# Kernel optimization log

Measured on AMD Instinct MI355X. Metric: run time of the kernel, lower is better.

Reference implementation:

```python
import jax, jax.numpy as jnp
import numpy as np

N = 100000   # nodes
E = 1000000  # edges (before self-loops)
G = 64       # graphs in batch
IN, HID, OUT = 128, 64, 1


def setup_inputs() -> dict:
    key = jax.random.key(0)
    ks = jax.random.split(key, 24)
    inp = {
        "x": jax.random.normal(ks[0], (N, IN), jnp.float32),
        "adj": jax.random.randint(ks[1], (2, E), 0, N, jnp.int32),
        "batch": jnp.sort(jax.random.randint(ks[2], (N,), 0, G, jnp.int32)),
    }
    i = 3
    dims = [(IN, HID), (HID, HID), (HID, HID)]
    for l, (di, do) in enumerate(dims, start=1):
        inp[f"W{l}"] = jax.random.normal(ks[i], (di, do), jnp.float32) * (1.0 / np.sqrt(di)); i += 1
        inp[f"a_src{l}"] = jax.random.normal(ks[i], (do,), jnp.float32) * 0.1; i += 1
        inp[f"a_dst{l}"] = jax.random.normal(ks[i], (do,), jnp.float32) * 0.1; i += 1
        inp[f"b{l}"] = jnp.zeros((do,), jnp.float32); i += 1
    inp["linnews_W"] = jax.random.normal(ks[i], (IN, HID), jnp.float32) * (1.0 / np.sqrt(IN)); i += 1
    inp["linnews_b"] = jnp.zeros((HID,), jnp.float32)
    inp["lin0_W"] = jax.random.normal(ks[i], (HID, HID), jnp.float32) * (1.0 / np.sqrt(HID)); i += 1
    inp["lin0_b"] = jnp.zeros((HID,), jnp.float32)
    inp["lin1_W"] = jax.random.normal(ks[i], (2 * HID, OUT), jnp.float32) * (1.0 / np.sqrt(2 * HID)); i += 1
    inp["lin1_b"] = jnp.zeros((OUT,), jnp.float32)
    return inp


def _gat_layer(x, src, dst, W, a_src, a_dst, b):
    # PyG GATConv, heads=1, self-loops already appended to (src, dst).
    h = x @ W                                        # [N, HID]
    e = (h @ a_src)[src] + (h @ a_dst)[dst]          # [E'] edge scores
    e = jax.nn.leaky_relu(e, 0.2)
    # segment softmax over incoming edges of each dst node
    m = jax.ops.segment_max(e, dst, num_segments=N)
    num = jnp.exp(e - m[dst])
    den = jax.ops.segment_sum(num, dst, num_segments=N)
    coef = num / (den[dst] + 1e-16)                  # [E']
    out = jax.ops.segment_sum(coef[:, None] * h[src], dst, num_segments=N)
    return out + b


def reference(x, adj, batch, W1, a_src1, a_dst1, b1, W2, a_src2, a_dst2, b2,
              W3, a_src3, a_dst3, b3, linnews_W, linnews_b, lin0_W, lin0_b,
              lin1_W, lin1_b):
    loop = jnp.arange(N, dtype=adj.dtype)
    src = jnp.concatenate([adj[0], loop])
    dst = jnp.concatenate([adj[1], loop])

    h = jax.nn.relu(_gat_layer(x, src, dst, W1, a_src1, a_dst1, b1))
    h = jax.nn.relu(_gat_layer(h, src, dst, W2, a_src2, a_dst2, b2))
    h = jax.nn.relu(_gat_layer(h, src, dst, W3, a_src3, a_dst3, b3))

    # global max pool per graph
    h = jax.ops.segment_max(h, batch, num_segments=G)        # [G, HID]
    h = jax.nn.relu(h @ lin0_W + lin0_b)

    # root node of each graph = first index with that batch id
    root = jax.ops.segment_min(jnp.arange(N), batch, num_segments=G)  # [G]
    news = jax.nn.relu(x[root] @ linnews_W + linnews_b)      # [G, HID]

    out = jnp.concatenate([h, news], axis=-1) @ lin1_W + lin1_b
    return jax.nn.sigmoid(out)                               # [G, 1]
```

## Files before the change

### kernel.cpp

```cpp
#include <hip/hip_runtime.h>
#include <hip/hip_fp16.h>
#include <cstdint>
#include <type_traits>

#define THREADS 256
#define NBLK 64
#define BPAD 512
#define LINBLK 640

typedef _Float16 half8 __attribute__((ext_vector_type(8)));
typedef float v4f __attribute__((ext_vector_type(4)));

__global__ __launch_bounds__(256) void hist_kernel(const int* __restrict__ dst_e,
                                                   int* __restrict__ hist, int E, int chunk,
                                                   float* __restrict__ pool, int* __restrict__ root,
                                                   int G) {
  __shared__ int hcnt[BPAD];
  int t = threadIdx.x, blk = blockIdx.x;
  if (blk == 0) {
    for (int i = t; i < G * 64; i += 256) pool[i] = 0.0f;
    for (int i = t; i < G; i += 256) root[i] = 0x7fffffff;
  }
  for (int i = t; i < BPAD; i += 256) hcnt[i] = 0;
  __syncthreads();
  int s = blk * chunk, e = s + chunk;
  if (e > E) e = E;
  for (int i = s + t; i < e; i += 256) atomicAdd(&hcnt[dst_e[i] >> 8], 1);
  __syncthreads();
  for (int b = t; b < BPAD; b += 256) hist[b * NBLK + blk] = hcnt[b];
}

__global__ __launch_bounds__(256) void hscan_kernel(int* __restrict__ hist) {
  __shared__ int part[256];
  const int PER = (BPAD * NBLK) / 256;
  int t = threadIdx.x;
  int base = t * PER;
  int sum = 0;
  for (int k = 0; k < PER; k++) sum += hist[base + k];
  part[t] = sum;
  __syncthreads();
  int own = sum;
  for (int off = 1; off < 256; off <<= 1) {
    int v = (t >= off) ? part[t - off] : 0;
    __syncthreads();
    part[t] += v;
    __syncthreads();
  }
  int run = part[t] - own;
  for (int k = 0; k < PER; k++) {
    int h = hist[base + k];
    hist[base + k] = run;
    run += h;
  }
}

__global__ __launch_bounds__(256) void scatter_kernel(const int* __restrict__ src_e,
                                                      const int* __restrict__ dst_e,
                                                      const int* __restrict__ hist,
                                                      unsigned int* __restrict__ ebuf,
                                                      int E, int chunk) {
  __shared__ int cur[BPAD];
  int t = threadIdx.x, blk = blockIdx.x;
  for (int b = t; b < BPAD; b += 256) cur[b] = hist[b * NBLK + blk];
  __syncthreads();
  int s = blk * chunk, e = s + chunk;
  if (e > E) e = E;
  for (int i = s + t; i < e; i += 256) {
    int d = dst_e[i];
    unsigned int sv = (unsigned int)src_e[i];
    int slot = atomicAdd(&cur[d >> 8], 1);
    ebuf[slot] = (sv << 8) | (unsigned int)(d & 255);
  }
}

__global__ __launch_bounds__(256) void build_kernel(const unsigned int* __restrict__ ebuf,
                                                    const int* __restrict__ hist,
                                                    int* __restrict__ row_start,
                                                    int* __restrict__ csr_src,
                                                    int N, int E) {
  __shared__ int counts[256];
  __shared__ int sc[256];
  __shared__ int curw[256];
  int t = threadIdx.x, b = blockIdx.x;
  int nbase = b * 256;
  int ebase = hist[b * NBLK];
  int eend = hist[(b + 1) * NBLK];
  counts[t] = 0;
  __syncthreads();
  int ecount = eend - ebase;
  for (int i = t; i < ecount; i += 256)
    atomicAdd(&counts[ebuf[ebase + i] & 255u], 1);
  __syncthreads();
  int n = nbase + t;
  int val = (n < N) ? counts[t] + 1 : 0;
  sc[t] = val;
  __syncthreads();
  int own = val;
  for (int off = 1; off < 256; off <<= 1) {
    int v = (t >= off) ? sc[t - off] : 0;
    __syncthreads();
    sc[t] += v;
    __syncthreads();
  }
  int myloc = sc[t] - own;
  int rowb = ebase + nbase;
  if (n < N) {
    row_start[n] = rowb + myloc;
    csr_src[rowb + myloc + counts[t]] = n;
    if (n == N - 1) row_start[N] = rowb + myloc + counts[t] + 1;
  }
  curw[t] = rowb + myloc;
  __syncthreads();
  for (int i = t; i < ecount; i += 256) {
    unsigned int ev = ebuf[ebase + i];
    int pos = atomicAdd(&curw[ev & 255u], 1);
    csr_src[pos] = (int)(ev >> 8);
  }
}

template <int K, typename TIN>
__global__ __launch_bounds__(256) void lin_attn_kernel(
    const TIN* __restrict__ in, const float* __restrict__ W,
    const float* __restrict__ a_src, const float* __restrict__ a_dst,
    __half2* __restrict__ h2, float* __restrict__ as_, float* __restrict__ ad_,
    int N, int nwaves) {
  constexpr int NKC = K / 32;
  __shared__ _Float16 sh[4][16 * 64];
  const int t = threadIdx.x;
  const int lane = t & 63, w = t >> 6;
  const int col = lane & 15, quad = lane >> 4;
  const int wid = blockIdx.x * 4 + w;

  half8 bf[4][NKC];
#pragma unroll
  for (int nt = 0; nt < 4; nt++)
#pragma unroll
    for (int kc = 0; kc < NKC; kc++) {
      half8 v;
#pragma unroll
      for (int j = 0; j < 8; j++)
        v[j] = (_Float16)W[(kc * 32 + quad * 8 + j) * 64 + nt * 16 + col];
      bf[nt][kc] = v;
    }
  float sa[4], sd[4];
#pragma unroll
  for (int nt = 0; nt < 4; nt++) {
    sa[nt] = a_src[nt * 16 + col];
    sd[nt] = a_dst[nt * 16 + col];
  }

  const int ntiles = (N + 15) >> 4;
  for (int tile = wid; tile < ntiles; tile += nwaves) {
    const int nb = tile << 4;
    int nodeA = nb + col;
    if (nodeA >= N) nodeA = N - 1;
    const TIN* arow = in + (size_t)nodeA * K + quad * 8;

    v4f acc[4];
#pragma unroll
    for (int nt = 0; nt < 4; nt++) acc[nt] = (v4f){0.f, 0.f, 0.f, 0.f};

#pragma unroll
    for (int kc = 0; kc < NKC; kc++) {
      half8 a;
      if constexpr (std::is_same<TIN, float>::value) {
        float4 f0 = *(const float4*)(arow + kc * 32);
        float4 f1 = *(const float4*)(arow + kc * 32 + 4);
        a[0] = (_Float16)f0.x; a[1] = (_Float16)f0.y;
        a[2] = (_Float16)f0.z; a[3] = (_Float16)f0.w;
        a[4] = (_Float16)f1.x; a[5] = (_Float16)f1.y;
        a[6] = (_Float16)f1.z; a[7] = (_Float16)f1.w;
      } else {
        a = *(const half8*)(arow + kc * 32);
      }
#pragma unroll
      for (int nt = 0; nt < 4; nt++)
        acc[nt] = __builtin_amdgcn_mfma_f32_16x16x32_f16(a, bf[nt][kc], acc[nt], 0, 0, 0);
    }

    float ps[4], pd[4];
#pragma unroll
    for (int r = 0; r < 4; r++) { ps[r] = 0.f; pd[r] = 0.f; }
#pragma unroll
    for (int nt = 0; nt < 4; nt++)
#pragma unroll
      for (int r = 0; r < 4; r++) {
        ps[r] += acc[nt][r] * sa[nt];
        pd[r] += acc[nt][r] * sd[nt];
      }
#pragma unroll
    for (int r = 0; r < 4; r++)
#pragma unroll
      for (int m = 1; m < 16; m <<= 1) {
        ps[r] += __shfl_xor(ps[r], m);
        pd[r] += __shfl_xor(pd[r], m);
      }
    if (col == 0) {
#pragma unroll
      for (int r = 0; r < 4; r++) {
        int node = nb + quad * 4 + r;
        if (node < N) { as_[node] = ps[r]; ad_[node] = pd[r]; }
      }
    }

#pragma unroll
    for (int nt = 0; nt < 4; nt++)
#pragma unroll
      for (int r = 0; r < 4; r++)
        sh[w][(quad * 4 + r) * 64 + nt * 16 + col] = (_Float16)acc[nt][r];
    int nr = lane >> 2, c4 = lane & 3;
    float4 v0 = *(float4*)&sh[w][nr * 64 + c4 * 16];
    float4 v1 = *(float4*)&sh[w][nr * 64 + c4 * 16 + 8];
    int node = nb + nr;
    if (node < N) {
      *(float4*)&h2[(size_t)node * 32 + c4 * 8] = v0;
      *(float4*)&h2[(size_t)node * 32 + c4 * 8 + 4] = v1;
    }
  }
}

__global__ __launch_bounds__(256) void agg_kernel(
    const __half2* __restrict__ h2, const float* __restrict__ as_, const float* __restrict__ ad_,
    const int* __restrict__ csr_src, const int* __restrict__ row_start,
    const float* __restrict__ b, _Float16* __restrict__ out16, int N) {
  int t = threadIdx.x;
  int lane = t & 63, w = t >> 6;
  int ng = lane >> 3, co = lane & 7;
  int n = blockIdx.x * 32 + w * 8 + ng;
  if (n >= N) return;
  int rs = row_start[n], re = row_start[n + 1];
  float adn = ad_[n];
  const float4* h4 = (const float4*)h2;

  float4 A0 = make_float4(0.f, 0.f, 0.f, 0.f);
  float4 A1 = make_float4(0.f, 0.f, 0.f, 0.f);
  float den = 0.f;
  for (int s = rs; s < re; s += 4) {
    int src[4];
#pragma unroll
    for (int j = 0; j < 4; j++) {
      int sj = s + j;
      src[j] = csr_src[(sj < re) ? sj : (re - 1)];
    }
    float cf[4];
#pragma unroll
    for (int j = 0; j < 4; j++) {
      float e = as_[src[j]] + adn;
      e = fmaxf(e, 0.2f * e);
      cf[j] = (s + j < re) ? __expf(e) : 0.f;
    }
#pragma unroll
    for (int j = 0; j < 4; j++) {
      float4 hv = h4[(size_t)src[j] * 8 + co];
      const __half2* hp = (const __half2*)&hv;
      float2 f0 = __half22float2(hp[0]);
      float2 f1 = __half22float2(hp[1]);
      float2 f2 = __half22float2(hp[2]);
      float2 f3 = __half22float2(hp[3]);
      float c = cf[j];
      den += c;
      A0.x += c * f0.x; A0.y += c * f0.y; A0.z += c * f1.x; A0.w += c * f1.y;
      A1.x += c * f2.x; A1.y += c * f2.y; A1.z += c * f3.x; A1.w += c * f3.y;
    }
  }
  float inv = 1.0f / (den + 1e-16f);
  float4 b0 = *(const float4*)&b[co * 8];
  float4 b1 = *(const float4*)&b[co * 8 + 4];
  _Float16 o[8];
  o[0] = (_Float16)fmaxf(A0.x * inv + b0.x, 0.f);
  o[1] = (_Float16)fmaxf(A0.y * inv + b0.y, 0.f);
  o[2] = (_Float16)fmaxf(A0.z * inv + b0.z, 0.f);
  o[3] = (_Float16)fmaxf(A0.w * inv + b0.w, 0.f);
  o[4] = (_Float16)fmaxf(A1.x * inv + b1.x, 0.f);
  o[5] = (_Float16)fmaxf(A1.y * inv + b1.y, 0.f);
  o[6] = (_Float16)fmaxf(A1.z * inv + b1.z, 0.f);
  o[7] = (_Float16)fmaxf(A1.w * inv + b1.w, 0.f);
  *(float4*)&out16[(size_t)n * 64 + co * 8] = *(float4*)o;
}

__global__ void pool_kernel(const _Float16* __restrict__ h, const int* __restrict__ batch,
                            float* __restrict__ pool, int* __restrict__ root,
                            int N, int chunk) {
  int t = threadIdx.x;
  int lane = t & 63, w = t >> 6;
  int row = blockIdx.x * 4 + w;
  int start = row * chunk;
  if (start >= N) return;
  int end = start + chunk; if (end > N) end = N;
  int cur_g = batch[start];
  if (lane == 0 && (start == 0 || batch[start - 1] != cur_g)) atomicMin(&root[cur_g], start);
  float rm = 0.0f;
  for (int n = start; n < end; n++) {
    int g = batch[n];
    if (g != cur_g) {
      atomicMax((int*)&pool[(size_t)cur_g * 64 + lane], __float_as_int(rm));
      if (lane == 0) atomicMin(&root[g], n);
      cur_g = g;
      rm = 0.0f;
    }
    rm = fmaxf(rm, (float)h[(size_t)n * 64 + lane]);
  }
  atomicMax((int*)&pool[(size_t)cur_g * 64 + lane], __float_as_int(rm));
}

__global__ void final_kernel(const float* __restrict__ pool, const int* __restrict__ root,
                             const float* __restrict__ x,
                             const float* __restrict__ lin0_W, const float* __restrict__ lin0_b,
                             const float* __restrict__ linnews_W, const float* __restrict__ linnews_b,
                             const float* __restrict__ lin1_W, const float* __restrict__ lin1_b,
                             float* __restrict__ out, int G, int N) {
  int t = threadIdx.x;
  int lane = t & 63, w = t >> 6;
  int g = blockIdx.x * 4 + w;
  if (g >= G) return;
  float hp = 0.f;
  for (int k = 0; k < 64; k++) hp += pool[(size_t)g * 64 + k] * lin0_W[k * 64 + lane];
  hp = fmaxf(hp + lin0_b[lane], 0.f);
  int r = root[g]; if (r > N - 1) r = N - 1; if (r < 0) r = 0;
  float nw = 0.f;
  for (int k = 0; k < 128; k++) nw += x[(size_t)r * 128 + k] * linnews_W[k * 64 + lane];
  nw = fmaxf(nw + linnews_b[lane], 0.f);
  float p = hp * lin1_W[lane] + nw * lin1_W[64 + lane];
  for (int k = 1; k < 64; k <<= 1) p += __shfl_xor(p, k);
  if (lane == 0) out[g] = 1.0f / (1.0f + __expf(-(p + lin1_b[0])));
}

extern "C" void kernel_launch(void* const* d_in, const int* in_sizes, int n_in,
                              void* d_out, int out_size, void* d_ws, size_t ws_size,
                              hipStream_t stream) {
  (void)n_in; (void)ws_size;
  const float* x      = (const float*)d_in[0];
  const int*   adj    = (const int*)d_in[1];
  const int*   batch  = (const int*)d_in[2];
  const float* W1     = (const float*)d_in[3];
  const float* asrc1  = (const float*)d_in[4];
  const float* adst1  = (const float*)d_in[5];
  const float* b1     = (const float*)d_in[6];
  const float* W2     = (const float*)d_in[7];
  const float* asrc2  = (const float*)d_in[8];
  const float* adst2  = (const float*)d_in[9];
  const float* b2     = (const float*)d_in[10];
  const float* W3     = (const float*)d_in[11];
  const float* asrc3  = (const float*)d_in[12];
  const float* adst3  = (const float*)d_in[13];
  const float* b3     = (const float*)d_in[14];
  const float* lnW    = (const float*)d_in[15];
  const float* lnb    = (const float*)d_in[16];
  const float* l0W    = (const float*)d_in[17];
  const float* l0b    = (const float*)d_in[18];
  const float* l1W    = (const float*)d_in[19];
  const float* l1b    = (const float*)d_in[20];
  float* outp = (float*)d_out;

  const int N = in_sizes[2];
  const int E = in_sizes[1] / 2;
  const int Etot = E + N;
  const int G = out_size;
  const int B = (N + 255) / 256;

  const int* src_e = adj;
  const int* dst_e = adj + E;

  uintptr_t p = (uintptr_t)d_ws;
  auto alloc = [&](size_t bytes) -> void* {
    void* r = (void*)p;
    p += (bytes + 255) & ~(size_t)255;
    return r;
  };
  int*      hist      = (int*)alloc((size_t)BPAD * NBLK * 4);
  int*      row_start = (int*)alloc((size_t)(N + 1) * 4);
  int*      csr_src   = (int*)alloc((size_t)Etot * 4);
  unsigned int* ebuf  = (unsigned int*)alloc((size_t)E * 4);
  __half2*  hbufL     = (__half2*)alloc((size_t)N * 32 * 4);
  _Float16* hbufA     = (_Float16*)alloc((size_t)N * 64 * 2);
  float*    as_       = (float*)alloc((size_t)N * 4);
  float*    ad_       = (float*)alloc((size_t)N * 4);
  float*    pool      = (float*)alloc((size_t)G * 64 * 4);
  int*      root      = (int*)alloc((size_t)G * 4);

  int chunk = (E + NBLK - 1) / NBLK;
  hist_kernel<<<dim3(NBLK), dim3(256), 0, stream>>>(dst_e, hist, E, chunk, pool, root, G);
  hscan_kernel<<<dim3(1), dim3(256), 0, stream>>>(hist);
  scatter_kernel<<<dim3(NBLK), dim3(256), 0, stream>>>(src_e, dst_e, hist, ebuf, E, chunk);
  build_kernel<<<dim3(B), dim3(256), 0, stream>>>(ebuf, hist, row_start, csr_src, N, E);

  const int aggGrid = (N + 31) / 32;
  const int nwaves = LINBLK * 4;

  lin_attn_kernel<128, float><<<dim3(LINBLK), dim3(256), 0, stream>>>(
      x, W1, asrc1, adst1, hbufL, as_, ad_, N, nwaves);
  agg_kernel<<<dim3(aggGrid), dim3(256), 0, stream>>>(hbufL, as_, ad_, csr_src, row_start, b1, hbufA, N);
  lin_attn_kernel<64, _Float16><<<dim3(LINBLK), dim3(256), 0, stream>>>(
      hbufA, W2, asrc2, adst2, hbufL, as_, ad_, N, nwaves);
  agg_kernel<<<dim3(aggGrid), dim3(256), 0, stream>>>(hbufL, as_, ad_, csr_src, row_start, b2, hbufA, N);
  lin_attn_kernel<64, _Float16><<<dim3(LINBLK), dim3(256), 0, stream>>>(
      hbufA, W3, asrc3, adst3, hbufL, as_, ad_, N, nwaves);
  agg_kernel<<<dim3(aggGrid), dim3(256), 0, stream>>>(hbufL, as_, ad_, csr_src, row_start, b3, hbufA, N);

  const int ROWS = 2048;
  int pchunk = (N + ROWS - 1) / ROWS;
  pool_kernel<<<dim3(ROWS / 4), dim3(256), 0, stream>>>(hbufA, batch, pool, root, N, pchunk);

  final_kernel<<<dim3((G + 3) / 4), dim3(256), 0, stream>>>(
      pool, root, x, l0W, l0b, lnW, lnb, l1W, l1b, outp, G, N);
}
```

Before: 325.2 us.

## Fuse GAT aggregation with next layer's linear+attention and final pooling

After: 309.4 us. 4.9% less time.

```diff
diff --git a/kernel.cpp b/kernel.cpp
--- a/kernel.cpp
+++ b/kernel.cpp
@@ -125,7 +125,7 @@
     __half2* __restrict__ h2, float* __restrict__ as_, float* __restrict__ ad_,
     int N, int nwaves) {
   constexpr int NKC = K / 32;
-  __shared__ _Float16 sh[4][16 * 64];
+  __shared__ _Float16 sh[4][16 * 72];
   const int t = threadIdx.x;
   const int lane = t & 63, w = t >> 6;
   const int col = lane & 15, quad = lane >> 4;
@@ -207,10 +207,10 @@
     for (int nt = 0; nt < 4; nt++)
 #pragma unroll
       for (int r = 0; r < 4; r++)
-        sh[w][(quad * 4 + r) * 64 + nt * 16 + col] = (_Float16)acc[nt][r];
+        sh[w][(quad * 4 + r) * 72 + nt * 16 + col] = (_Float16)acc[nt][r];
     int nr = lane >> 2, c4 = lane & 3;
-    float4 v0 = *(float4*)&sh[w][nr * 64 + c4 * 16];
-    float4 v1 = *(float4*)&sh[w][nr * 64 + c4 * 16 + 8];
+    float4 v0 = *(float4*)&sh[w][nr * 72 + c4 * 16];
+    float4 v1 = *(float4*)&sh[w][nr * 72 + c4 * 16 + 8];
     int node = nb + nr;
     if (node < N) {
       *(float4*)&h2[(size_t)node * 32 + c4 * 8] = v0;
@@ -219,22 +219,11 @@
   }
 }
 
-__global__ __launch_bounds__(256) void agg_kernel(
-    const __half2* __restrict__ h2, const float* __restrict__ as_, const float* __restrict__ ad_,
-    const int* __restrict__ csr_src, const int* __restrict__ row_start,
-    const float* __restrict__ b, _Float16* __restrict__ out16, int N) {
-  int t = threadIdx.x;
-  int lane = t & 63, w = t >> 6;
-  int ng = lane >> 3, co = lane & 7;
-  int n = blockIdx.x * 32 + w * 8 + ng;
-  if (n >= N) return;
-  int rs = row_start[n], re = row_start[n + 1];
-  float adn = ad_[n];
-  const float4* h4 = (const float4*)h2;
-
-  float4 A0 = make_float4(0.f, 0.f, 0.f, 0.f);
-  float4 A1 = make_float4(0.f, 0.f, 0.f, 0.f);
-  float den = 0.f;
+__device__ __forceinline__ void agg_node(const float4* __restrict__ h4,
+                                         const float* __restrict__ as_in, float adn,
+                                         const int* __restrict__ csr_src,
+                                         int rs, int re, int co,
+                                         float4& A0, float4& A1, float& den) {
   for (int s = rs; s < re; s += 4) {
     int src[4];
 #pragma unroll
@@ -245,7 +234,7 @@
     float cf[4];
 #pragma unroll
     for (int j = 0; j < 4; j++) {
-      float e = as_[src[j]] + adn;
+      float e = as_in[src[j]] + adn;
       e = fmaxf(e, 0.2f * e);
       cf[j] = (s + j < re) ? __expf(e) : 0.f;
     }
@@ -263,44 +252,179 @@
       A1.x += c * f2.x; A1.y += c * f2.y; A1.z += c * f3.x; A1.w += c * f3.y;
     }
   }
+}
+
+__global__ __launch_bounds__(256) void agg_lin_kernel(
+    const __half2* __restrict__ h2in, const float* __restrict__ as_in,
+    const float* __restrict__ ad_in, const int* __restrict__ csr_src,
+    const int* __restrict__ row_start, const float* __restrict__ bprev,
+    const float* __restrict__ W, const float* __restrict__ a_src,
+    const float* __restrict__ a_dst, __half2* __restrict__ h2out,
+    float* __restrict__ as_out, float* __restrict__ ad_out, int N) {
+  __shared__ _Float16 shh[32][72];
+  __shared__ _Float16 sht[2][16 * 72];
+  const int t = threadIdx.x;
+  const int lane = t & 63, w = t >> 6;
+
+  {
+    const int ng = lane >> 3, co = lane & 7;
+    const int ln = w * 8 + ng;
+    int n = blockIdx.x * 32 + ln;
+    int nc = (n < N) ? n : (N - 1);
+    int rs = row_start[nc], re = row_start[nc + 1];
+    float adn = ad_in[nc];
+    const float4* h4 = (const float4*)h2in;
+    float4 A0 = make_float4(0.f, 0.f, 0.f, 0.f);
+    float4 A1 = make_float4(0.f, 0.f, 0.f, 0.f);
+    float den = 0.f;
+    agg_node(h4, as_in, adn, csr_src, rs, re, co, A0, A1, den);
+    float inv = 1.0f / (den + 1e-16f);
+    float4 b0 = *(const float4*)&bprev[co * 8];
+    float4 b1 = *(const float4*)&bprev[co * 8 + 4];
+    _Float16 o[8];
+    o[0] = (_Float16)fmaxf(A0.x * inv + b0.x, 0.f);
+    o[1] = (_Float16)fmaxf(A0.y * inv + b0.y, 0.f);
+    o[2] = (_Float16)fmaxf(A0.z * inv + b0.z, 0.f);
+    o[3] = (_Float16)fmaxf(A0.w * inv + b0.w, 0.f);
+    o[4] = (_Float16)fmaxf(A1.x * inv + b1.x, 0.f);
+    o[5] = (_Float16)fmaxf(A1.y * inv + b1.y, 0.f);
+    o[6] = (_Float16)fmaxf(A1.z * inv + b1.z, 0.f);
+    o[7] = (_Float16)fmaxf(A1.w * inv + b1.w, 0.f);
+    *(float4*)&shh[ln][co * 8] = *(float4*)o;
+  }
+  __syncthreads();
+  if (w >= 2) return;
+
+  const int col = lane & 15, quad = lane >> 4;
+  half8 bf[4][2];
+  float sa[4], sd[4];
+#pragma unroll
+  for (int nt = 0; nt < 4; nt++) {
+#pragma unroll
+    for (int kc = 0; kc < 2; kc++) {
+      half8 v;
+#pragma unroll
+      for (int j = 0; j < 8; j++)
+        v[j] = (_Float16)W[(kc * 32 + quad * 8 + j) * 64 + nt * 16 + col];
+      bf[nt][kc] = v;
+    }
+    sa[nt] = a_src[nt * 16 + col];
+    sd[nt] = a_dst[nt * 16 + col];
+  }
+
+  const int nb = blockIdx.x * 32 + w * 16;
+  v4f acc[4];
+#pragma unroll
+  for (int nt = 0; nt < 4; nt++) acc[nt] = (v4f){0.f, 0.f, 0.f, 0.f};
+#pragma unroll
+  for (int kc = 0; kc < 2; kc++) {
+    half8 a = *(const half8*)&shh[w * 16 + col][kc * 32 + quad * 8];
+#pragma unroll
+    for (int nt = 0; nt < 4; nt++)
+      acc[nt] = __builtin_amdgcn_mfma_f32_16x16x32_f16(a, bf[nt][kc], acc[nt], 0, 0, 0);
+  }
+
+  float ps[4], pd[4];
+#pragma unroll
+  for (int r = 0; r < 4; r++) { ps[r] = 0.f; pd[r] = 0.f; }
+#pragma unroll
+  for (int nt = 0; nt < 4; nt++)
+#pragma unroll
+    for (int r = 0; r < 4; r++) {
+      ps[r] += acc[nt][r] * sa[nt];
+      pd[r] += acc[nt][r] * sd[nt];
+    }
+#pragma unroll
+  for (int r = 0; r < 4; r++)
+#pragma unroll
+    for (int m = 1; m < 16; m <<= 1) {
+      ps[r] += __shfl_xor(ps[r], m);
+      pd[r] += __shfl_xor(pd[r], m);
+    }
+  if (col == 0) {
+#pragma unroll
+    for (int r = 0; r < 4; r++) {
+      int node = nb + quad * 4 + r;
+      if (node < N) { as_out[node] = ps[r]; ad_out[node] = pd[r]; }
+    }
+  }
+
+#pragma unroll
+  for (int nt = 0; nt < 4; nt++)
+#pragma unroll
+    for (int r = 0; r < 4; r++)
+      sht[w][(quad * 4 + r) * 72 + nt * 16 + col] = (_Float16)acc[nt][r];
+  int nr = lane >> 2, c4 = lane & 3;
+  float4 v0 = *(float4*)&sht[w][nr * 72 + c4 * 16];
+  float4 v1 = *(float4*)&sht[w][nr * 72 + c4 * 16 + 8];
+  int node = nb + nr;
+  if (node < N) {
+    *(float4*)&h2out[(size_t)node * 32 + c4 * 8] = v0;
+    *(float4*)&h2out[(size_t)node * 32 + c4 * 8 + 4] = v1;
+  }
+}
+
+__global__ __launch_bounds__(256) void agg_pool_kernel(
+    const __half2* __restrict__ h2in, const float* __restrict__ as_in,
+    const float* __restrict__ ad_in, const int* __restrict__ csr_src,
+    const int* __restrict__ row_start, const float* __restrict__ bprev,
+    const int* __restrict__ batch, float* __restrict__ pool,
+    int* __restrict__ root, int N) {
+  __shared__ float red[4][64];
+  const int t = threadIdx.x;
+  const int lane = t & 63, w = t >> 6;
+  const int ng = lane >> 3, co = lane & 7;
+  const int ln = w * 8 + ng;
+  int n = blockIdx.x * 32 + ln;
+  int nc = (n < N) ? n : (N - 1);
+  int rs = row_start[nc], re = row_start[nc + 1];
+  float adn = ad_in[nc];
+  const float4* h4 = (const float4*)h2in;
+  float4 A0 = make_float4(0.f, 0.f, 0.f, 0.f);
+  float4 A1 = make_float4(0.f, 0.f, 0.f, 0.f);
+  float den = 0.f;
+  agg_node(h4, as_in, adn, csr_src, rs, re, co, A0, A1, den);
   float inv = 1.0f / (den + 1e-16f);
-  float4 b0 = *(const float4*)&b[co * 8];
-  float4 b1 = *(const float4*)&b[co * 8 + 4];
-  _Float16 o[8];
-  o[0] = (_Float16)fmaxf(A0.x * inv + b0.x, 0.f);
-  o[1] = (_Float16)fmaxf(A0.y * inv + b0.y, 0.f);
-  o[2] = (_Float16)fmaxf(A0.z * inv + b0.z, 0.f);
-  o[3] = (_Float16)fmaxf(A0.w * inv + b0.w, 0.f);
-  o[4] = (_Float16)fmaxf(A1.x * inv + b1.x, 0.f);
-  o[5] = (_Float16)fmaxf(A1.y * inv + b1.y, 0.f);
-  o[6] = (_Float16)fmaxf(A1.z * inv + b1.z, 0.f);
-  o[7] = (_Float16)fmaxf(A1.w * inv + b1.w, 0.f);
-  *(float4*)&out16[(size_t)n * 64 + co * 8] = *(float4*)o;
-}
-
-__global__ void pool_kernel(const _Float16* __restrict__ h, const int* __restrict__ batch,
-                            float* __restrict__ pool, int* __restrict__ root,
-                            int N, int chunk) {
-  int t = threadIdx.x;
-  int lane = t & 63, w = t >> 6;
-  int row = blockIdx.x * 4 + w;
-  int start = row * chunk;
-  if (start >= N) return;
-  int end = start + chunk; if (end > N) end = N;
-  int cur_g = batch[start];
-  if (lane == 0 && (start == 0 || batch[start - 1] != cur_g)) atomicMin(&root[cur_g], start);
-  float rm = 0.0f;
-  for (int n = start; n < end; n++) {
-    int g = batch[n];
-    if (g != cur_g) {
-      atomicMax((int*)&pool[(size_t)cur_g * 64 + lane], __float_as_int(rm));
-      if (lane == 0) atomicMin(&root[g], n);
-      cur_g = g;
-      rm = 0.0f;
-    }
-    rm = fmaxf(rm, (float)h[(size_t)n * 64 + lane]);
-  }
-  atomicMax((int*)&pool[(size_t)cur_g * 64 + lane], __float_as_int(rm));
+  float4 b0 = *(const float4*)&bprev[co * 8];
+  float4 b1 = *(const float4*)&bprev[co * 8 + 4];
+  float ov[8];
+  ov[0] = (float)(_Float16)fmaxf(A0.x * inv + b0.x, 0.f);
+  ov[1] = (float)(_Float16)fmaxf(A0.y * inv + b0.y, 0.f);
+  ov[2] = (float)(_Float16)fmaxf(A0.z * inv + b0.z, 0.f);
+  ov[3] = (float)(_Float16)fmaxf(A0.w * inv + b0.w, 0.f);
+  ov[4] = (float)(_Float16)fmaxf(A1.x * inv + b1.x, 0.f);
+  ov[5] = (float)(_Float16)fmaxf(A1.y * inv + b1.y, 0.f);
+  ov[6] = (float)(_Float16)fmaxf(A1.z * inv + b1.z, 0.f);
+  ov[7] = (float)(_Float16)fmaxf(A1.w * inv + b1.w, 0.f);
+
+  int g = batch[nc];
+  if (co == 0 && n < N) {
+    if (n == 0 || batch[n - 1] != g) atomicMin(&root[g], n);
+  }
+
+  int bstart = blockIdx.x * 32;
+  int bend = bstart + 31; if (bend >= N) bend = N - 1;
+  int gfirst = batch[bstart];
+  int glast = batch[bend];
+  if (gfirst == glast) {
+#pragma unroll
+    for (int m = 8; m < 64; m <<= 1)
+#pragma unroll
+      for (int j = 0; j < 8; j++) ov[j] = fmaxf(ov[j], __shfl_xor(ov[j], m));
+    if (ng == 0)
+#pragma unroll
+      for (int j = 0; j < 8; j++) red[w][co * 8 + j] = ov[j];
+    __syncthreads();
+    if (t < 64) {
+      float m0 = fmaxf(red[0][t], red[1][t]);
+      float m1 = fmaxf(red[2][t], red[3][t]);
+      atomicMax((int*)&pool[(size_t)gfirst * 64 + t], __float_as_int(fmaxf(m0, m1)));
+    }
+  } else {
+#pragma unroll
+    for (int j = 0; j < 8; j++)
+      if (n < N) atomicMax((int*)&pool[(size_t)g * 64 + co * 8 + j], __float_as_int(ov[j]));
+  }
 }
 
 __global__ void final_kernel(const float* __restrict__ pool, const int* __restrict__ root,
@@ -371,10 +495,12 @@
   int*      row_start = (int*)alloc((size_t)(N + 1) * 4);
   int*      csr_src   = (int*)alloc((size_t)Etot * 4);
   unsigned int* ebuf  = (unsigned int*)alloc((size_t)E * 4);
-  __half2*  hbufL     = (__half2*)alloc((size_t)N * 32 * 4);
-  _Float16* hbufA     = (_Float16*)alloc((size_t)N * 64 * 2);
-  float*    as_       = (float*)alloc((size_t)N * 4);
-  float*    ad_       = (float*)alloc((size_t)N * 4);
+  __half2*  hA        = (__half2*)alloc((size_t)N * 32 * 4);
+  __half2*  hB        = (__half2*)alloc((size_t)N * 32 * 4);
+  float*    asA       = (float*)alloc((size_t)N * 4);
+  float*    adA       = (float*)alloc((size_t)N * 4);
+  float*    asB       = (float*)alloc((size_t)N * 4);
+  float*    adB       = (float*)alloc((size_t)N * 4);
   float*    pool      = (float*)alloc((size_t)G * 64 * 4);
   int*      root      = (int*)alloc((size_t)G * 4);
 
@@ -388,18 +514,13 @@
   const int nwaves = LINBLK * 4;
 
   lin_attn_kernel<128, float><<<dim3(LINBLK), dim3(256), 0, stream>>>(
-      x, W1, asrc1, adst1, hbufL, as_, ad_, N, nwaves);
-  agg_kernel<<<dim3(aggGrid), dim3(256), 0, stream>>>(hbufL, as_, ad_, csr_src, row_start, b1, hbufA, N);
-  lin_attn_kernel<64, _Float16><<<dim3(LINBLK), dim3(256), 0, stream>>>(
-      hbufA, W2, asrc2, adst2, hbufL, as_, ad_, N, nwaves);
-  agg_kernel<<<dim3(aggGrid), dim3(256), 0, stream>>>(hbufL, as_, ad_, csr_src, row_start, b2, hbufA, N);
-  lin_attn_kernel<64, _Float16><<<dim3(LINBLK), dim3(256), 0, stream>>>(
-      hbufA, W3, asrc3, adst3, hbufL, as_, ad_, N, nwaves);
-  agg_kernel<<<dim3(aggGrid), dim3(256), 0, stream>>>(hbufL, as_, ad_, csr_src, row_start, b3, hbufA, N);
-
-  const int ROWS = 2048;
-  int pchunk = (N + ROWS - 1) / ROWS;
-  pool_kernel<<<dim3(ROWS / 4), dim3(256), 0, stream>>>(hbufA, batch, pool, root, N, pchunk);
+      x, W1, asrc1, adst1, hA, asA, adA, N, nwaves);
+  agg_lin_kernel<<<dim3(aggGrid), dim3(256), 0, stream>>>(
+      hA, asA, adA, csr_src, row_start, b1, W2, asrc2, adst2, hB, asB, adB, N);
+  agg_lin_kernel<<<dim3(aggGrid), dim3(256), 0, stream>>>(
+      hB, asB, adB, csr_src, row_start, b2, W3, asrc3, adst3, hA, asA, adA, N);
+  agg_pool_kernel<<<dim3(aggGrid), dim3(256), 0, stream>>>(
+      hA, asA, adA, csr_src, row_start, b3, batch, pool, root, N);
 
   final_kernel<<<dim3((G + 3) / 4), dim3(256), 0, stream>>>(
       pool, root, x, l0W, l0b, lnW, lnb, l1W, l1b, outp, G, N);
```
